# Kernel tuning notes

Measured on AMD Instinct MI355X. Metric: run time of the kernel, lower is better.

## Reference

```python
import itertools
import jax, jax.numpy as jnp
import numpy as np

B, S, D = 256, 49, 448          # batch, tokens (7x7), channels
H, KD, ED = 8, 32, 128          # heads, key_dim, expanded_key_dim (attn_ratio*key_dim)
QKV_OUT = H * (KD + KD + ED)    # 1536
MLP_HID = 4 * D                 # 1792
EPS = 1e-12
SCALE = KD ** -0.5


def _bias_idxs(resolution=7):
    points = list(itertools.product(range(resolution), range(resolution)))
    offsets, idxs = {}, []
    for p1 in points:
        for p2 in points:
            off = (abs(p1[0] - p2[0]), abs(p1[1] - p2[1]))
            if off not in offsets:
                offsets[off] = len(offsets)
            idxs.append(offsets[off])
    n = len(points)
    return np.asarray(idxs, np.int32).reshape(n, n), len(offsets)


def setup_inputs() -> dict:
    key = jax.random.key(0)
    ks = jax.random.split(key, 12)
    idxs_np, n_off = _bias_idxs(7)  # [49,49], 49 offsets
    s = 0.02
    return {
        "hidden_states": jax.random.normal(ks[0], (B, S, D), jnp.float32),
        "ln2_w": jnp.ones((D,), jnp.float32),
        "ln2_b": jnp.zeros((D,), jnp.float32),
        "qkv_w": jax.random.normal(ks[1], (QKV_OUT, D), jnp.float32) * s,
        "qkv_b": jnp.zeros((QKV_OUT,), jnp.float32),
        "proj_w": jax.random.normal(ks[2], (D, H * ED), jnp.float32) * s,
        "proj_b": jnp.zeros((D,), jnp.float32),
        "attention_biases": jax.random.normal(ks[3], (H, n_off), jnp.float32) * s,
        "fc1_w": jax.random.normal(ks[4], (MLP_HID, D), jnp.float32) * s,
        "fc1_b": jnp.zeros((MLP_HID,), jnp.float32),
        "fc2_w": jax.random.normal(ks[5], (D, MLP_HID), jnp.float32) * s,
        "fc2_b": jnp.zeros((D,), jnp.float32),
        "layer_scale_1": jnp.full((D,), 1e-5, jnp.float32),
        "layer_scale_2": jnp.full((D,), 1e-5, jnp.float32),
        "attention_bias_idxs": jnp.asarray(idxs_np),  # int32 [49,49]
    }


def _layernorm(x, w, b):
    mu = jnp.mean(x, axis=-1, keepdims=True)
    var = jnp.mean(jnp.square(x - mu), axis=-1, keepdims=True)
    return (x - mu) * jax.lax.rsqrt(var + EPS) * w + b


def reference(hidden_states, ln2_w, ln2_b, qkv_w, qkv_b, proj_w, proj_b,
              attention_biases, fc1_w, fc1_b, fc2_w, fc2_b,
              layer_scale_1, layer_scale_2, attention_bias_idxs):
    # NOTE: upstream code applies norm2 before BOTH attention and MLP (faithful).
    norm = _layernorm(hidden_states, ln2_w, ln2_b)  # [B,S,D]

    qkv = (norm @ qkv_w.T + qkv_b).reshape(B, S, H, KD + KD + ED)
    q, k, v = jnp.split(qkv, [KD, 2 * KD], axis=-1)  # [B,S,H,KD/KD/ED]

    bias = attention_biases[:, attention_bias_idxs]  # [H,S,S] gathered rel-pos bias
    scores = jnp.einsum("bqhd,bkhd->bhqk", q, k) * SCALE + bias[None]
    probs = jax.nn.softmax(scores, axis=-1)          # [B,H,S,S]

    ctx = jnp.einsum("bhqk,bkhd->bqhd", probs, v).reshape(B, S, H * ED)
    attn_out = ctx @ proj_w.T + proj_b               # [B,S,D]

    out = hidden_states + layer_scale_1 * attn_out
    mlp = jax.nn.gelu(norm @ fc1_w.T + fc1_b, approximate=False) @ fc2_w.T + fc2_b
    out = out + layer_scale_2 * mlp
    return out
```

## Files before the change

kernel.cpp:

```cpp
#include <hip/hip_runtime.h>
#include <hip/hip_bf16.h>
#include <cstdint>

#define B_    256
#define S_    49
#define D_    448
#define H_    8
#define KD_   32
#define ED_   128
#define NTOK  (B_*S_)
#define QKVO  1536
#define MLPH  1792
#define SCALE_ 0.17677669529663687f

using bf16x8  = __attribute__((ext_vector_type(8))) __bf16;
using ushort8 = __attribute__((ext_vector_type(8))) unsigned short;
using f32x4   = __attribute__((ext_vector_type(4))) float;

__device__ __forceinline__ unsigned short f2bf(float f){
  uint32_t u = __builtin_bit_cast(uint32_t, f);
  u += 0x7fffu + ((u >> 16) & 1u);
  return (unsigned short)(u >> 16);
}
__device__ __forceinline__ float b2f(unsigned short b){
  uint32_t u = ((uint32_t)b) << 16;
  return __builtin_bit_cast(float, u);
}

__device__ __forceinline__ void gload_lds16(const void* g, void* l){
  __builtin_amdgcn_global_load_lds(
      (const __attribute__((address_space(1))) void*)g,
      (__attribute__((address_space(3))) void*)l, 16, 0, 0);
}

#define P_S0 688128L
#define P_S1 1490944L
#define P_S2 1949696L
#define P_S3 2752512L
#define P_S4 2932736L
#define P_S5 2936064L
#define P_S6 2936576L
#define P_S7 2969344L
__global__ __launch_bounds__(256)
void prep_k(const float* __restrict__ qkvw, const float* __restrict__ fc1w,
            const float* __restrict__ projw, const float* __restrict__ fc2w,
            const float* __restrict__ ls1, const float* __restrict__ ls2,
            const float* __restrict__ qkvb, const float* __restrict__ fc1b,
            const float* __restrict__ projb, const float* __restrict__ fc2b,
            const float* __restrict__ attb, const int* __restrict__ idxs,
            unsigned short* __restrict__ wcat, unsigned short* __restrict__ wfused,
            float* __restrict__ cbig, float* __restrict__ cbv,
            float* __restrict__ biasf){
  const long i = (long)blockIdx.x * 256 + threadIdx.x;
  if (i < P_S0){
    wcat[i] = f2bf(qkvw[i]);
  } else if (i < P_S1){
    long j = i - P_S0;
    wcat[i] = f2bf(fc1w[j]);
  } else if (i < P_S2){
    long j = i - P_S1;
    long r = j / 1024, c = j - r*1024;
    wfused[r*2816 + c] = f2bf(projw[j]*ls1[r]);
  } else if (i < P_S3){
    long j = i - P_S2;
    long r = j / 1792, c = j - r*1792;
    wfused[r*2816 + 1024 + c] = f2bf(fc2w[j]*ls2[r]);
  } else if (i < P_S4){
    long j = i - P_S3;
    wfused[448L*2816 + j] = 0;
  } else if (i < P_S5){
    long j = i - P_S4;
    cbig[j] = (j < 1536) ? qkvb[j] : fc1b[j - 1536];
  } else if (i < P_S6){
    long j = i - P_S5;
    cbv[j] = (j < 448) ? ls1[j]*projb[j] + ls2[j]*fc2b[j] : 0.f;
  } else if (i < P_S7){
    long j = i - P_S6;
    int h = (int)(j >> 12), r = (int)((j >> 6) & 63), c = (int)(j & 63);
    float v;
    if (c >= 49) v = -1e30f;
    else { int q = r < 49 ? r : 48; v = attb[h*49 + idxs[q*49 + c]]; }
    biasf[j] = v;
  }
}

__global__ __launch_bounds__(448)
void ln_k(const float* __restrict__ x, const float* __restrict__ w,
          const float* __restrict__ b, unsigned short* __restrict__ out){
  const int tok = blockIdx.x, t = threadIdx.x;
  const float v = x[(size_t)tok*448 + t];
  float s1 = v, s2 = v*v;
  #pragma unroll
  for (int o = 32; o; o >>= 1){ s1 += __shfl_xor(s1, o); s2 += __shfl_xor(s2, o); }
  __shared__ float a1[7], a2[7];
  const int wid = t >> 6;
  if ((t & 63) == 0){ a1[wid] = s1; a2[wid] = s2; }
  __syncthreads();
  float S1 = 0.f, S2 = 0.f;
  #pragma unroll
  for (int i = 0; i < 7; ++i){ S1 += a1[i]; S2 += a2[i]; }
  const float mu  = S1 * (1.f/448.f);
  const float var = S2 * (1.f/448.f) - mu*mu;
  const float rs  = rsqrtf(var + 1e-12f);
  out[(size_t)tok*448 + t] = f2bf((v - mu)*rs*w[t] + b[t]);
}

template<int EPI>
__global__ __launch_bounds__(256)
void gemm_k(const unsigned short* __restrict__ A1, int lda1, int nkt1,
            const unsigned short* __restrict__ A2, int lda2, int nkt,
            const unsigned short* __restrict__ W, int ldw,
            const float* __restrict__ bias,
            const float* __restrict__ resid, float* __restrict__ outF,
            unsigned short* __restrict__ outB1, int ldo1,
            unsigned short* __restrict__ outB2, int ldo2, int splitBy)
{
  __shared__ char smem[65536];
  unsigned short* const As0 = (unsigned short*)smem;
  unsigned short* const As1 = As0 + 8192;
  unsigned short* const Bs0 = As1 + 8192;
  unsigned short* const Bs1 = Bs0 + 8192;

  const int t = threadIdx.x, lane = t & 63, wid = t >> 6;
  const int wm = wid >> 1, wn = wid & 1;
  const int g = lane >> 4, li = lane & 15;
  const int bx = blockIdx.x, by = blockIdx.y;
  f32x4 acc[4][4] = {};

  const int srow  = lane >> 3;
  const int scolw = ((lane & 7) ^ srow) * 8;

  auto stage = [&](unsigned short* As, unsigned short* Bs, int kt){
    const unsigned short* Ab; int lda, k0;
    if (kt < nkt1){ Ab = A1; lda = lda1; k0 = kt*64; }
    else          { Ab = A2; lda = lda2; k0 = (kt - nkt1)*64; }
    #pragma unroll
    for (int i = 0; i < 4; ++i){
      const int c = wid*4 + i;
      gload_lds16(Ab + (size_t)(bx*128 + c*8 + srow)*lda + k0 + scolw, As + c*512);
    }
    #pragma unroll
    for (int i = 0; i < 4; ++i){
      const int c = wid*4 + i;
      gload_lds16(W + (size_t)(by*128 + c*8 + srow)*ldw + kt*64 + scolw, Bs + c*512);
    }
  };

  unsigned short *Asc = As0, *Asn = As1, *Bsc = Bs0, *Bsn = Bs1;
  stage(Asc, Bsc, 0);
  for (int kt = 0; kt < nkt; ++kt){
    __syncthreads();
    if (kt + 1 < nkt) stage(Asn, Bsn, kt + 1);
    #pragma unroll
    for (int ks = 0; ks < 2; ++ks){
      const int kk2 = (ks*32 + g*8)*2;
      bf16x8 af[4], bfr[4];
      #pragma unroll
      for (int mf = 0; mf < 4; ++mf){
        const int row = wm*64 + mf*16 + li;
        af[mf] = *reinterpret_cast<const bf16x8*>(
            (char*)Asc + row*128 + (kk2 ^ ((row & 7) << 4)));
      }
      #pragma unroll
      for (int nf = 0; nf < 4; ++nf){
        const int row = wn*64 + nf*16 + li;
        bfr[nf] = *reinterpret_cast<const bf16x8*>(
            (char*)Bsc + row*128 + (kk2 ^ ((row & 7) << 4)));
      }
      #pragma unroll
      for (int mf = 0; mf < 4; ++mf)
        #pragma unroll
        for (int nf = 0; nf < 4; ++nf)
          acc[mf][nf] = __builtin_amdgcn_mfma_f32_16x16x32_bf16(af[mf], bfr[nf], acc[mf][nf], 0, 0, 0);
    }
    { unsigned short* tmp = Asc; Asc = Asn; Asn = tmp; }
    { unsigned short* tmp = Bsc; Bsc = Bsn; Bsn = tmp; }
  }
  __syncthreads();

  const bool dogelu = (EPI == 4) && (by >= splitBy);
  #pragma unroll
  for (int mf = 0; mf < 4; ++mf){
    #pragma unroll
    for (int nf = 0; nf < 4; ++nf){
      const int col = wn*64 + nf*16 + li;
      const float bi = bias[by*128 + col];
      #pragma unroll
      for (int j = 0; j < 4; ++j){
        const int row = wm*64 + mf*16 + g*4 + j;
        float v = acc[mf][nf][j] + bi;
        if (dogelu) v = 0.5f*v*(1.0f + erff(v*0.70710678118654752f));
        *reinterpret_cast<float*>(smem + row*512 + ((col*4) ^ (((row >> 2) & 3) << 6))) = v;
      }
    }
  }
  __syncthreads();

  const int lr = lane >> 4, lc = lane & 15;
  if (EPI == 4){
    #pragma unroll
    for (int it = 0; it < 8; ++it){
      const int r = wid*32 + it*4 + lr;
      const int sw = ((r >> 2) & 3) << 6;
      const f32x4 v0 = *reinterpret_cast<const f32x4*>(smem + r*512 + ((lc*32)      ^ sw));
      const f32x4 v1 = *reinterpret_cast<const f32x4*>(smem + r*512 + ((lc*32 + 16) ^ sw));
      ushort8 u;
      #pragma unroll
      for (int k = 0; k < 4; ++k){ u[k] = f2bf(v0[k]); u[4+k] = f2bf(v1[k]); }
      const int grow = bx*128 + r;
      if (by < splitBy)
        *reinterpret_cast<ushort8*>(outB1 + (size_t)grow*ldo1 + by*128 + lc*8) = u;
      else
        *reinterpret_cast<ushort8*>(outB2 + (size_t)grow*ldo2 + by*128 - splitBy*128 + lc*8) = u;
    }
  } else {
    #pragma unroll
    for (int i = 0; i < 8; ++i){
      const int r = wid*32 + i*4 + lr;
      const int sw = ((r >> 2) & 3) << 6;
      #pragma unroll
      for (int half = 0; half < 2; ++half){
        const int colb = half*64 + lc*4;
        const int gcol = by*128 + colb;
        if (gcol < 448){
          const f32x4 v = *reinterpret_cast<const f32x4*>(smem + r*512 + ((colb*4) ^ sw));
          const size_t o = (size_t)(bx*128 + r)*448 + gcol;
          const f32x4 rs = *reinterpret_cast<const f32x4*>(resid + o);
          *reinterpret_cast<f32x4*>(outF + o) = rs + v;
        }
      }
    }
  }
}

__global__ __launch_bounds__(256)
void attn_mfma_k(const unsigned short* __restrict__ qkv,
                 const float* __restrict__ biasf,
                 unsigned short* __restrict__ ctx)
{
  const int bh = blockIdx.x;
  const int b = bh >> 3, h = bh & 7;
  __shared__ unsigned short Vs[64*128];
  __shared__ unsigned short Ps[64*64];
  const int t = threadIdx.x, lane = t & 63, w = t >> 6;
  const int g = lane >> 4, li = lane & 15;
  const size_t qbase = ((size_t)b*49)*QKVO + (size_t)h*192;

  for (int c = t; c < 64*16; c += 256){
    const int k = c >> 4, seg = c & 15;
    bf16x8 v = {};
    if (k < 49)
      v = *reinterpret_cast<const bf16x8*>(qkv + qbase + 64 + (size_t)k*QKVO + seg*8);
    const int byte = (k*256 + seg*16) ^ ((((unsigned)k >> 3) & 3) << 5);
    *reinterpret_cast<bf16x8*>((char*)Vs + byte) = v;
  }

  const int qrow = w*16 + li;
  bf16x8 afq = {};
  if (qrow < 49)
    afq = *reinterpret_cast<const bf16x8*>(qkv + qbase + (size_t)qrow*QKVO + g*8);
  f32x4 accs[4];
  #pragma unroll
  for (int nf = 0; nf < 4; ++nf){
    const int krow = nf*16 + li;
    bf16x8 bfr = {};
    if (krow < 49)
      bfr = *reinterpret_cast<const bf16x8*>(qkv + qbase + 32 + (size_t)krow*QKVO + g*8);
    f32x4 z = {};
    accs[nf] = __builtin_amdgcn_mfma_f32_16x16x32_bf16(afq, bfr, z, 0, 0, 0);
  }

  #pragma unroll
  for (int j = 0; j < 4; ++j){
    const int row = w*16 + g*4 + j;
    float sv[4];
    #pragma unroll
    for (int nf = 0; nf < 4; ++nf)
      sv[nf] = accs[nf][j]*SCALE_ + biasf[h*4096 + row*64 + nf*16 + li];
    float m = fmaxf(fmaxf(sv[0], sv[1]), fmaxf(sv[2], sv[3]));
    #pragma unroll
    for (int o = 8; o; o >>= 1) m = fmaxf(m, __shfl_xor(m, o));
    float e[4], s = 0.f;
    #pragma unroll
    for (int nf = 0; nf < 4; ++nf){ e[nf] = __expf(sv[nf] - m); s += e[nf]; }
    #pragma unroll
    for (int o = 8; o; o >>= 1) s += __shfl_xor(s, o);
    const float inv = 1.f / s;
    #pragma unroll
    for (int nf = 0; nf < 4; ++nf){
      const int byte = (row*128 + (nf*16 + li)*2) ^ ((row & 7) << 4);
      *reinterpret_cast<unsigned short*>((char*)Ps + byte) = f2bf(e[nf]*inv);
    }
  }
  __syncthreads();

  f32x4 accp[4][2] = {};
  #pragma unroll
  for (int kt = 0; kt < 2; ++kt){
    bf16x8 pa[4];
    #pragma unroll
    for (int mt = 0; mt < 4; ++mt){
      const int q = mt*16 + li;
      const int byte = (q*128 + kt*64 + g*16) ^ ((q & 7) << 4);
      pa[mt] = *reinterpret_cast<const bf16x8*>((char*)Ps + byte);
    }
    #pragma unroll
    for (int nf = 0; nf < 2; ++nf){
      const int d = w*32 + nf*16 + li;
      ushort8 vbu;
      #pragma unroll
      for (int j = 0; j < 8; ++j){
        const int k = kt*32 + g*8 + j;
        const int byte = (k*256 + d*2) ^ ((((unsigned)k >> 3) & 3) << 5);
        vbu[j] = *reinterpret_cast<const unsigned short*>((char*)Vs + byte);
      }
      const bf16x8 vb = __builtin_bit_cast(bf16x8, vbu);
      #pragma unroll
      for (int mt = 0; mt < 4; ++mt)
        accp[mt][nf] = __builtin_amdgcn_mfma_f32_16x16x32_bf16(pa[mt], vb, accp[mt][nf], 0, 0, 0);
    }
  }

  const size_t obase = ((size_t)b*49)*1024 + (size_t)h*128;
  #pragma unroll
  for (int mt = 0; mt < 4; ++mt){
    #pragma unroll
    for (int nf = 0; nf < 2; ++nf){
      #pragma unroll
      for (int j = 0; j < 4; ++j){
        const int row = mt*16 + g*4 + j;
        if (row < 49){
          const int col = w*32 + nf*16 + li;
          ctx[obase + (size_t)row*1024 + col] = f2bf(accp[mt][nf][j]);
        }
      }
    }
  }
}

extern "C" void kernel_launch(void* const* d_in, const int* in_sizes, int n_in,
                              void* d_out, int out_size, void* d_ws, size_t ws_size,
                              hipStream_t stream)
{
  const float* hidden = (const float*)d_in[0];
  const float* ln2w   = (const float*)d_in[1];
  const float* ln2b   = (const float*)d_in[2];
  const float* qkvw   = (const float*)d_in[3];
  const float* qkvb   = (const float*)d_in[4];
  const float* projw  = (const float*)d_in[5];
  const float* projb  = (const float*)d_in[6];
  const float* attb   = (const float*)d_in[7];
  const float* fc1w   = (const float*)d_in[8];
  const float* fc1b   = (const float*)d_in[9];
  const float* fc2w   = (const float*)d_in[10];
  const float* fc2b   = (const float*)d_in[11];
  const float* ls1    = (const float*)d_in[12];
  const float* ls2    = (const float*)d_in[13];
  const int*   aidx   = (const int*)d_in[14];
  float* out = (float*)d_out;

  char* p = (char*)d_ws;
  auto alloc = [&](size_t bytes){ void* r = (void*)p; p += (bytes + 255) & ~(size_t)255; return r; };
  unsigned short* wcat   = (unsigned short*)alloc((size_t)3328*448*2);
  unsigned short* wfused = (unsigned short*)alloc((size_t)512*2816*2);
  unsigned short* normb  = (unsigned short*)alloc((size_t)NTOK*448*2);
  unsigned short* qkvv   = (unsigned short*)alloc((size_t)NTOK*QKVO*2);
  unsigned short* ctx    = (unsigned short*)alloc((size_t)NTOK*1024*2);
  unsigned short* hid    = (unsigned short*)alloc((size_t)NTOK*MLPH*2);
  float*          biasf  = (float*)alloc((size_t)8*64*64*4);
  float*          cbig   = (float*)alloc((size_t)3328*4);
  float*          cbv    = (float*)alloc((size_t)512*4);

  prep_k<<<(int)(P_S7/256), 256, 0, stream>>>(qkvw, fc1w, projw, fc2w, ls1, ls2,
                                              qkvb, fc1b, projb, fc2b, attb, aidx,
                                              wcat, wfused, cbig, cbv, biasf);
  ln_k<<<NTOK, 448, 0, stream>>>(hidden, ln2w, ln2b, normb);

  gemm_k<4><<<dim3(98,26), 256, 0, stream>>>(normb, 448, 7, nullptr, 448, 7,
                                             wcat, 448, cbig,
                                             nullptr, nullptr,
                                             qkvv, QKVO, hid, MLPH, 12);
  attn_mfma_k<<<B_*H_, 256, 0, stream>>>(qkvv, biasf, ctx);
  gemm_k<1><<<dim3(98,4), 256, 0, stream>>>(ctx, 1024, 16, hid, MLPH, 44,
                                            wfused, 2816, cbv,
                                            hidden, out,
                                            nullptr, 0, nullptr, 0, 999);
}
```

Before: 174.9 us.

## Shrink GEMM K-tile, narrow output GEMM tiles, add XCD-aware block remap

The GEMM kernel now uses a 32-wide K step with a new LDS swizzle, which cuts shared memory from 64KB to 32KB so more blocks can be resident per CU. The output GEMM switches to 128x64 tiles, so 7 column tiles exactly cover 448 columns and no blocks are wasted on columns past 448. A 1D grid with an XCD-aware block-id remap is added to improve L2 locality across the chiplets. In exchange there are twice as many K iterations and barriers, and the GELU epilogue is split into two passes, each followed by an extra barrier.

Result: slower. 181.6 us (+3.8%).

```diff
diff --git a/kernel.cpp b/kernel.cpp
--- a/kernel.cpp
+++ b/kernel.cpp
@@ -6,8 +6,6 @@
 #define S_    49
 #define D_    448
 #define H_    8
-#define KD_   32
-#define ED_   128
 #define NTOK  (B_*S_)
 #define QKVO  1536
 #define MLPH  1792
@@ -113,122 +111,143 @@
             const float* __restrict__ bias,
             const float* __restrict__ resid, float* __restrict__ outF,
             unsigned short* __restrict__ outB1, int ldo1,
-            unsigned short* __restrict__ outB2, int ldo2, int splitBy)
+            unsigned short* __restrict__ outB2, int ldo2,
+            int splitBy, int nby)
 {
-  __shared__ char smem[65536];
-  unsigned short* const As0 = (unsigned short*)smem;
-  unsigned short* const As1 = As0 + 8192;
-  unsigned short* const Bs0 = As1 + 8192;
-  unsigned short* const Bs1 = Bs0 + 8192;
+  constexpr int BN = (EPI == 4) ? 128 : 64;
+  constexpr int NF = BN/32;
+  __shared__ char smem[32768];
+
+  const int NB = gridDim.x;
+  const int q8 = NB >> 3, r8 = NB & 7;
+  const int xcd = blockIdx.x & 7, idx = blockIdx.x >> 3;
+  const int wgid = (xcd < r8 ? xcd*(q8+1) : r8*(q8+1) + (xcd-r8)*q8) + idx;
+  const int bx = wgid / nby, by = wgid - bx*nby;
 
   const int t = threadIdx.x, lane = t & 63, wid = t >> 6;
   const int wm = wid >> 1, wn = wid & 1;
   const int g = lane >> 4, li = lane & 15;
-  const int bx = blockIdx.x, by = blockIdx.y;
-  f32x4 acc[4][4] = {};
-
-  const int srow  = lane >> 3;
-  const int scolw = ((lane & 7) ^ srow) * 8;
-
-  auto stage = [&](unsigned short* As, unsigned short* Bs, int kt){
+  f32x4 acc[4][NF] = {};
+
+  const int l3   = lane >> 3;
+  const int sp   = (lane & 7) ^ l3;
+  const int rofs = 2*l3 + (sp >> 2);
+  const int cofs = (sp & 3)*8;
+
+  auto stage = [&](int buf, int kt){
+    char* Asb = smem + buf*8192;
+    char* Bsb = smem + 16384 + buf*(BN*64);
     const unsigned short* Ab; int lda, k0;
-    if (kt < nkt1){ Ab = A1; lda = lda1; k0 = kt*64; }
-    else          { Ab = A2; lda = lda2; k0 = (kt - nkt1)*64; }
-    #pragma unroll
-    for (int i = 0; i < 4; ++i){
-      const int c = wid*4 + i;
-      gload_lds16(Ab + (size_t)(bx*128 + c*8 + srow)*lda + k0 + scolw, As + c*512);
-    }
-    #pragma unroll
-    for (int i = 0; i < 4; ++i){
-      const int c = wid*4 + i;
-      gload_lds16(W + (size_t)(by*128 + c*8 + srow)*ldw + kt*64 + scolw, Bs + c*512);
+    if (kt < nkt1){ Ab = A1; lda = lda1; k0 = kt*32; }
+    else          { Ab = A2; lda = lda2; k0 = (kt - nkt1)*32; }
+    #pragma unroll
+    for (int i = 0; i < 2; ++i){
+      const int c = wid*2 + i;
+      gload_lds16(Ab + (size_t)(bx*128 + c*16 + rofs)*lda + k0 + cofs,
+                  Asb + c*1024);
+    }
+    if (BN == 128){
+      #pragma unroll
+      for (int i = 0; i < 2; ++i){
+        const int c = wid*2 + i;
+        gload_lds16(W + (size_t)(by*BN + c*16 + rofs)*ldw + kt*32 + cofs,
+                    Bsb + c*1024);
+      }
+    } else {
+      gload_lds16(W + (size_t)(by*BN + wid*16 + rofs)*ldw + kt*32 + cofs,
+                  Bsb + wid*1024);
     }
   };
 
-  unsigned short *Asc = As0, *Asn = As1, *Bsc = Bs0, *Bsn = Bs1;
-  stage(Asc, Bsc, 0);
+  const int sOff = (li >> 1)*128 + ((((li & 1)*4 + g) ^ (li >> 1)) << 4);
+
+  int buf = 0;
+  stage(0, 0);
   for (int kt = 0; kt < nkt; ++kt){
     __syncthreads();
-    if (kt + 1 < nkt) stage(Asn, Bsn, kt + 1);
-    #pragma unroll
-    for (int ks = 0; ks < 2; ++ks){
-      const int kk2 = (ks*32 + g*8)*2;
-      bf16x8 af[4], bfr[4];
-      #pragma unroll
-      for (int mf = 0; mf < 4; ++mf){
-        const int row = wm*64 + mf*16 + li;
-        af[mf] = *reinterpret_cast<const bf16x8*>(
-            (char*)Asc + row*128 + (kk2 ^ ((row & 7) << 4)));
-      }
-      #pragma unroll
-      for (int nf = 0; nf < 4; ++nf){
-        const int row = wn*64 + nf*16 + li;
-        bfr[nf] = *reinterpret_cast<const bf16x8*>(
-            (char*)Bsc + row*128 + (kk2 ^ ((row & 7) << 4)));
-      }
-      #pragma unroll
-      for (int mf = 0; mf < 4; ++mf)
-        #pragma unroll
-        for (int nf = 0; nf < 4; ++nf)
-          acc[mf][nf] = __builtin_amdgcn_mfma_f32_16x16x32_bf16(af[mf], bfr[nf], acc[mf][nf], 0, 0, 0);
-    }
-    { unsigned short* tmp = Asc; Asc = Asn; Asn = tmp; }
-    { unsigned short* tmp = Bsc; Bsc = Bsn; Bsn = tmp; }
-  }
-  __syncthreads();
-
-  const bool dogelu = (EPI == 4) && (by >= splitBy);
-  #pragma unroll
-  for (int mf = 0; mf < 4; ++mf){
-    #pragma unroll
-    for (int nf = 0; nf < 4; ++nf){
-      const int col = wn*64 + nf*16 + li;
-      const float bi = bias[by*128 + col];
-      #pragma unroll
-      for (int j = 0; j < 4; ++j){
-        const int row = wm*64 + mf*16 + g*4 + j;
-        float v = acc[mf][nf][j] + bi;
-        if (dogelu) v = 0.5f*v*(1.0f + erff(v*0.70710678118654752f));
-        *reinterpret_cast<float*>(smem + row*512 + ((col*4) ^ (((row >> 2) & 3) << 6))) = v;
-      }
-    }
+    if (kt + 1 < nkt) stage(buf ^ 1, kt + 1);
+    char* Asb = smem + buf*8192;
+    char* Bsb = smem + 16384 + buf*(BN*64);
+    bf16x8 af[4], bfr[NF];
+    #pragma unroll
+    for (int mf = 0; mf < 4; ++mf)
+      af[mf] = *reinterpret_cast<const bf16x8*>(Asb + wm*4096 + mf*1024 + sOff);
+    #pragma unroll
+    for (int nf = 0; nf < NF; ++nf)
+      bfr[nf] = *reinterpret_cast<const bf16x8*>(Bsb + wn*(BN*32) + nf*1024 + sOff);
+    #pragma unroll
+    for (int mf = 0; mf < 4; ++mf)
+      #pragma unroll
+      for (int nf = 0; nf < NF; ++nf)
+        acc[mf][nf] = __builtin_amdgcn_mfma_f32_16x16x32_bf16(af[mf], bfr[nf], acc[mf][nf], 0, 0, 0);
+    buf ^= 1;
   }
   __syncthreads();
 
   const int lr = lane >> 4, lc = lane & 15;
   if (EPI == 4){
-    #pragma unroll
-    for (int it = 0; it < 8; ++it){
-      const int r = wid*32 + it*4 + lr;
-      const int sw = ((r >> 2) & 3) << 6;
-      const f32x4 v0 = *reinterpret_cast<const f32x4*>(smem + r*512 + ((lc*32)      ^ sw));
-      const f32x4 v1 = *reinterpret_cast<const f32x4*>(smem + r*512 + ((lc*32 + 16) ^ sw));
-      ushort8 u;
-      #pragma unroll
-      for (int k = 0; k < 4; ++k){ u[k] = f2bf(v0[k]); u[4+k] = f2bf(v1[k]); }
-      const int grow = bx*128 + r;
-      if (by < splitBy)
-        *reinterpret_cast<ushort8*>(outB1 + (size_t)grow*ldo1 + by*128 + lc*8) = u;
-      else
-        *reinterpret_cast<ushort8*>(outB2 + (size_t)grow*ldo2 + by*128 - splitBy*128 + lc*8) = u;
+    const bool dogelu = by >= splitBy;
+    #pragma unroll
+    for (int p = 0; p < 2; ++p){
+      if (p) __syncthreads();
+      if (wm == p){
+        #pragma unroll
+        for (int mf = 0; mf < 4; ++mf){
+          #pragma unroll
+          for (int nf = 0; nf < NF; ++nf){
+            const int col = wn*64 + nf*16 + li;
+            const float bi = bias[by*128 + col];
+            #pragma unroll
+            for (int j = 0; j < 4; ++j){
+              const int rt = mf*16 + g*4 + j;
+              float v = acc[mf][nf][j] + bi;
+              if (dogelu) v = 0.5f*v*(1.0f + erff(v*0.70710678118654752f));
+              *reinterpret_cast<float*>(smem + rt*512 + ((col*4) ^ (((rt >> 2) & 3) << 6))) = v;
+            }
+          }
+        }
+      }
+      __syncthreads();
+      #pragma unroll
+      for (int it = 0; it < 4; ++it){
+        const int rt = wid*16 + it*4 + lr;
+        const int sw = ((rt >> 2) & 3) << 6;
+        const f32x4 v0 = *reinterpret_cast<const f32x4*>(smem + rt*512 + ((lc*32)      ^ sw));
+        const f32x4 v1 = *reinterpret_cast<const f32x4*>(smem + rt*512 + ((lc*32 + 16) ^ sw));
+        ushort8 u;
+        #pragma unroll
+        for (int k = 0; k < 4; ++k){ u[k] = f2bf(v0[k]); u[4+k] = f2bf(v1[k]); }
+        const int grow = bx*128 + p*64 + rt;
+        if (by < splitBy)
+          *reinterpret_cast<ushort8*>(outB1 + (size_t)grow*ldo1 + by*128 + lc*8) = u;
+        else
+          *reinterpret_cast<ushort8*>(outB2 + (size_t)grow*ldo2 + (by - splitBy)*128 + lc*8) = u;
+      }
     }
   } else {
+    #pragma unroll
+    for (int mf = 0; mf < 4; ++mf){
+      #pragma unroll
+      for (int nf = 0; nf < NF; ++nf){
+        const int col = wn*32 + nf*16 + li;
+        const float bi = bias[by*64 + col];
+        #pragma unroll
+        for (int j = 0; j < 4; ++j){
+          const int rt = wm*64 + mf*16 + g*4 + j;
+          *reinterpret_cast<float*>(smem + rt*256 + ((col*4) ^ (((rt >> 2) & 1) << 6)))
+              = acc[mf][nf][j] + bi;
+        }
+      }
+    }
+    __syncthreads();
     #pragma unroll
     for (int i = 0; i < 8; ++i){
       const int r = wid*32 + i*4 + lr;
-      const int sw = ((r >> 2) & 3) << 6;
-      #pragma unroll
-      for (int half = 0; half < 2; ++half){
-        const int colb = half*64 + lc*4;
-        const int gcol = by*128 + colb;
-        if (gcol < 448){
-          const f32x4 v = *reinterpret_cast<const f32x4*>(smem + r*512 + ((colb*4) ^ sw));
-          const size_t o = (size_t)(bx*128 + r)*448 + gcol;
-          const f32x4 rs = *reinterpret_cast<const f32x4*>(resid + o);
-          *reinterpret_cast<f32x4*>(outF + o) = rs + v;
-        }
-      }
+      const int sw = ((r >> 2) & 1) << 6;
+      const f32x4 v = *reinterpret_cast<const f32x4*>(smem + r*256 + ((lc*16) ^ sw));
+      const size_t o = (size_t)(bx*128 + r)*448 + by*64 + lc*4;
+      const f32x4 rs = *reinterpret_cast<const f32x4*>(resid + o);
+      *reinterpret_cast<f32x4*>(outF + o) = rs + v;
     }
   }
 }
@@ -376,13 +395,13 @@
                                               wcat, wfused, cbig, cbv, biasf);
   ln_k<<<NTOK, 448, 0, stream>>>(hidden, ln2w, ln2b, normb);
 
-  gemm_k<4><<<dim3(98,26), 256, 0, stream>>>(normb, 448, 7, nullptr, 448, 7,
-                                             wcat, 448, cbig,
-                                             nullptr, nullptr,
-                                             qkvv, QKVO, hid, MLPH, 12);
+  gemm_k<4><<<98*26, 256, 0, stream>>>(normb, 448, 14, nullptr, 448, 14,
+                                       wcat, 448, cbig,
+                                       nullptr, nullptr,
+                                       qkvv, QKVO, hid, MLPH, 12, 26);
   attn_mfma_k<<<B_*H_, 256, 0, stream>>>(qkvv, biasf, ctx);
-  gemm_k<1><<<dim3(98,4), 256, 0, stream>>>(ctx, 1024, 16, hid, MLPH, 44,
-                                            wfused, 2816, cbv,
-                                            hidden, out,
-                                            nullptr, 0, nullptr, 0, 999);
-}
+  gemm_k<1><<<98*7, 256, 0, stream>>>(ctx, 1024, 32, hid, MLPH, 88,
+                                      wfused, 2816, cbv,
+                                      hidden, out,
+                                      nullptr, 0, nullptr, 0, 999, 7);
+}
```
